# Performance work log

Hardware: AMD Instinct MI355X
Metric: run time of the kernel (lower is better)

## Reference

```python
import jax, jax.numpy as jnp
import numpy as np

B, N, K = 2, 8192, 16
C_IN, C_OUT = 32, 64
EPS = 1e-6


def _bn(x, g, b, axes):
    m = jnp.mean(x, axes, keepdims=True)
    v = jnp.var(x, axes, keepdims=True)
    return (x - m) * jax.lax.rsqrt(v + EPS) * g + b


def _leaky(x, s):
    return jnp.where(x >= 0, x, s * x)


def _knn(coords, k):
    # brute-force euclidean KNN, self point included (dist 0)
    sq = jnp.sum(coords * coords, -1)  # (B,N)
    d2 = sq[:, :, None] + sq[:, None, :] - 2.0 * jnp.einsum('bnd,bmd->bnm', coords, coords)
    neg, idx = jax.lax.top_k(-d2, k)  # (B,N,K)
    dist = jnp.sqrt(jnp.clip(-neg, 1e-12, None))
    return idx, dist


def setup_inputs() -> dict:
    key = jax.random.key(0)
    ks = jax.random.split(key, 12)
    h = C_OUT // 2
    w = lambda k, s: jax.random.normal(k, s, jnp.float32) * 0.05
    return {
        'coords': jax.random.normal(ks[0], (B, N, 3), jnp.float32),
        'features': jax.random.normal(ks[1], (B, N, C_IN), jnp.float32),
        'W_mlp1': w(ks[2], (C_IN, h)), 'b_mlp1': jnp.zeros(h, jnp.float32),
        'W_lse1': w(ks[3], (10, h)), 'b_lse1': jnp.zeros(h, jnp.float32),
        'g_lse1': jnp.ones(h, jnp.float32), 'be_lse1': jnp.zeros(h, jnp.float32),
        'W_att1_lin': w(ks[4], (C_OUT, C_OUT)),
        'W_att1_mlp': w(ks[5], (C_OUT, h)), 'b_att1_mlp': jnp.zeros(h, jnp.float32),
        'g_att1': jnp.ones(h, jnp.float32), 'be_att1': jnp.zeros(h, jnp.float32),
        'W_lse2': w(ks[6], (10, h)), 'b_lse2': jnp.zeros(h, jnp.float32),
        'g_lse2': jnp.ones(h, jnp.float32), 'be_lse2': jnp.zeros(h, jnp.float32),
        'W_att2_lin': w(ks[7], (C_OUT, C_OUT)),
        'W_att2_mlp': w(ks[8], (C_OUT, C_OUT)), 'b_att2_mlp': jnp.zeros(C_OUT, jnp.float32),
        'g_att2': jnp.ones(C_OUT, jnp.float32), 'be_att2': jnp.zeros(C_OUT, jnp.float32),
        'W_mlp2': w(ks[9], (C_OUT, 2 * C_OUT)), 'b_mlp2': jnp.zeros(2 * C_OUT, jnp.float32),
        'W_short': w(ks[10], (C_IN, 2 * C_OUT)), 'b_short': jnp.zeros(2 * C_OUT, jnp.float32),
        'g_short': jnp.ones(2 * C_OUT, jnp.float32), 'be_short': jnp.zeros(2 * C_OUT, jnp.float32),
    }


def _forward(coords, features, W_mlp1, b_mlp1, W_lse1, b_lse1, g_lse1, be_lse1,
             W_att1_lin, W_att1_mlp, b_att1_mlp, g_att1, be_att1,
             W_lse2, b_lse2, g_lse2, be_lse2,
             W_att2_lin, W_att2_mlp, b_att2_mlp, g_att2, be_att2,
             W_mlp2, b_mlp2, W_short, b_short, g_short, be_short):
    idx, dist = _knn(coords, K)                     # (B,N,K)
    nbr = jax.vmap(lambda c, i: c[i])(coords, idx)  # gather neighbor coords (B,N,K,3)
    center = jnp.broadcast_to(coords[:, :, None, :], nbr.shape)
    # spatial encoding: [center, neighbor, center-neighbor, dist] -> 10 channels
    se = jnp.concatenate([center, nbr, center - nbr, dist[..., None]], -1)  # (B,N,K,10)

    # mlp1 (1x1 conv + LeakyReLU(0.2)), no BN
    x = _leaky(features @ W_mlp1 + b_mlp1, 0.2)     # (B,N,h)

    # LocSE 1: shared MLP (BN train-mode + ReLU) on spatial enc, concat features
    sp1 = jax.nn.relu(_bn(se @ W_lse1 + b_lse1, g_lse1, be_lse1, (0, 1, 2)))  # (B,N,K,h)
    x1 = jnp.concatenate([sp1, jnp.broadcast_to(x[:, :, None, :], sp1.shape)], -1)  # (B,N,K,2h)

    # attention pooling 1: softmax over neighbors K, weighted sum, MLP+BN+ReLU
    sc1 = jax.nn.softmax(x1 @ W_att1_lin, axis=2)
    p1 = jnp.sum(sc1 * x1, axis=2)                  # (B,N,2h)
    x = jax.nn.relu(_bn(p1 @ W_att1_mlp + b_att1_mlp, g_att1, be_att1, (0, 1)))  # (B,N,h)

    # LocSE 2 + attention pooling 2 (same KNN, separate weights)
    sp2 = jax.nn.relu(_bn(se @ W_lse2 + b_lse2, g_lse2, be_lse2, (0, 1, 2)))
    x2 = jnp.concatenate([sp2, jnp.broadcast_to(x[:, :, None, :], sp2.shape)], -1)
    sc2 = jax.nn.softmax(x2 @ W_att2_lin, axis=2)
    p2 = jnp.sum(sc2 * x2, axis=2)
    x = jax.nn.relu(_bn(p2 @ W_att2_mlp + b_att2_mlp, g_att2, be_att2, (0, 1)))  # (B,N,C_OUT)

    # mlp2 (no BN, no act) + shortcut (BN, no act), residual LeakyReLU(0.01)
    x = x @ W_mlp2 + b_mlp2                          # (B,N,2*C_OUT)
    short = _bn(features @ W_short + b_short, g_short, be_short, (0, 1))
    out = _leaky(x + short, 0.01)
    # match torch layout (B, 2*C_OUT, N, 1)
    return jnp.transpose(out, (0, 2, 1))[..., None]


def reference(coords, features, W_mlp1, b_mlp1, W_lse1, b_lse1, g_lse1, be_lse1,
              W_att1_lin, W_att1_mlp, b_att1_mlp, g_att1, be_att1,
              W_lse2, b_lse2, g_lse2, be_lse2,
              W_att2_lin, W_att2_mlp, b_att2_mlp, g_att2, be_att2,
              W_mlp2, b_mlp2, W_short, b_short, g_short, be_short):
    return _forward(coords, features, W_mlp1, b_mlp1, W_lse1, b_lse1, g_lse1, be_lse1,
                    W_att1_lin, W_att1_mlp, b_att1_mlp, g_att1, be_att1,
                    W_lse2, b_lse2, g_lse2, be_lse2,
                    W_att2_lin, W_att2_mlp, b_att2_mlp, g_att2, be_att2,
                    W_mlp2, b_mlp2, W_short, b_short, g_short, be_short)
```

## Files before the change

kernel.cpp:

```cpp
#include <hip/hip_runtime.h>
#include <cfloat>
#include <cmath>

#define DEV __device__ __forceinline__

constexpr int BB = 2, NN = 8192, KK = 16, CIN = 32, HH = 32, CO = 64, C2 = 128;
constexpr int BNTOT = BB * NN;
constexpr int BNKROWS = BB * NN * KK;
constexpr float EPSF = 1e-6f;

constexpr int S_LSE1 = 0, S_LSE2 = 64, S_ATT1 = 128, S_ATT2 = 192, S_SHORT = 320, S_TOTAL = 576;
constexpr int SS_LSE1 = 0, SS_LSE2 = 64, SS_ATT1 = 128, SS_ATT2 = 192, SS_SHORT = 320, SS_TOTAL = 576;

constexpr size_t OFF_CP4   = 0;
constexpr size_t OFF_SE    = OFF_CP4 + (size_t)BNTOT * 4;
constexpr size_t OFF_XF    = OFF_SE + (size_t)BNKROWS * 10;
constexpr size_t OFF_SHORT = OFF_XF + (size_t)BNTOT * HH;
constexpr size_t OFF_PRE1  = OFF_SHORT + (size_t)BNTOT * C2;
constexpr size_t OFF_PRE2  = OFF_PRE1 + (size_t)BNTOT * HH;
constexpr size_t OFF_SS    = OFF_PRE2 + (size_t)BNTOT * CO;
constexpr size_t OFF_STATS = OFF_SS + SS_TOTAL;

__global__ __launch_bounds__(256) void k_prep(const float* __restrict__ coords,
                                              float4* __restrict__ cp4) {
#pragma clang fp contract(off)
    int i = blockIdx.x * 256 + threadIdx.x;
    if (i >= BNTOT) return;
    float x = coords[3 * i], y = coords[3 * i + 1], z = coords[3 * i + 2];
    float sq = (x * x + y * y) + z * z;
    cp4[i] = make_float4(x, y, z, sq);
}

DEV float dist2(float4 qc, float4 c) {
#pragma clang fp contract(off)
    float dot = (qc.x * c.x + qc.y * c.y) + qc.z * c.z;
    return (qc.w + c.w) - 2.0f * dot;
}

DEV unsigned encf(float f) {
    unsigned u = __float_as_uint(f);
    return (u & 0x80000000u) ? ~u : (u | 0x80000000u);
}
DEV float decf(unsigned e) {
    unsigned u = (e & 0x80000000u) ? (e & 0x7FFFFFFFu) : ~e;
    return __uint_as_float(u);
}

DEV void ins16(float (&dl)[16], int (&il)[16], float d, int id) {
    float dk = d; int jk = id;
#pragma unroll
    for (int r = 0; r < 16; ++r) {
        bool c = dk < dl[r];
        float td = dl[r]; int ti = il[r];
        dl[r] = c ? dk : dl[r]; il[r] = c ? jk : il[r];
        dk = c ? td : dk; jk = c ? ti : jk;
    }
}

DEV void ins16_lex(float (&dl)[16], int (&il)[16], float d, int id) {
    float dk = d; int jk = id;
#pragma unroll
    for (int r = 0; r < 16; ++r) {
        bool c = (dk < dl[r]) || (dk == dl[r] && jk < il[r]);
        float td = dl[r]; int ti = il[r];
        dl[r] = c ? dk : dl[r]; il[r] = c ? jk : il[r];
        dk = c ? td : dk; jk = c ? ti : jk;
    }
}

__global__ __launch_bounds__(256) void k_knn(const float4* __restrict__ cp4,
                                             float* __restrict__ se) {
    __shared__ uint2 buf[7][256];
    __shared__ float mdl[8][32][17];
    __shared__ int   mil[8][32][17];
    __shared__ unsigned thr[32];

    int t = threadIdx.x;
    int b = blockIdx.x >> 8;
    int qbase = (blockIdx.x & 255) * 32;
    int ql = t & 31, part = t >> 5;
    const float4* cp = cp4 + (size_t)b * NN;
    float4 qc = cp[qbase + ql];

    if (t < 32) thr[t] = encf(FLT_MAX);
    __syncthreads();

    float dl[16]; int il[16];
#pragma unroll
    for (int i = 0; i < 16; ++i) { dl[i] = FLT_MAX; il[i] = 0; }

    int cb = part * 1024;
#pragma unroll
    for (int k = 0; k < 16; ++k) ins16(dl, il, dist2(qc, cp[cb + k]), cb + k);
    atomicMin(&thr[ql], encf(dl[15]));
    float Tf = dl[15];
    int cnt = 0;

    float4 n0 = cp[cb + 16], n1 = cp[cb + 17], n2 = cp[cb + 18], n3 = cp[cb + 19];
    unsigned te = thr[ql];
    for (int j = cb + 16; j < cb + 1024; j += 4) {
        float4 c0 = n0, c1 = n1, c2 = n2, c3 = n3;
        n0 = cp[j + 4]; n1 = cp[j + 5]; n2 = cp[j + 6]; n3 = cp[j + 7];
        float d0 = dist2(qc, c0), d1 = dist2(qc, c1), d2v = dist2(qc, c2), d3 = dist2(qc, c3);
        bool p0 = d0 <= Tf, p1 = d1 <= Tf, p2 = d2v <= Tf, p3 = d3 <= Tf;
        if (__any(p0 | p1 | p2 | p3)) {
            if (p0) { buf[cnt][t] = make_uint2(__float_as_uint(d0), (unsigned)(j)); ++cnt; }
            if (p1) { buf[cnt][t] = make_uint2(__float_as_uint(d1), (unsigned)(j + 1)); ++cnt; }
            if (p2) { buf[cnt][t] = make_uint2(__float_as_uint(d2v), (unsigned)(j + 2)); ++cnt; }
            if (p3) { buf[cnt][t] = make_uint2(__float_as_uint(d3), (unsigned)(j + 3)); ++cnt; }
            if (__any(cnt >= 4)) {
#pragma unroll
                for (int s = 0; s < 7; ++s) {
                    if (s < cnt) {
                        uint2 v = buf[s][t];
                        float d = __uint_as_float(v.x);
                        if (d < dl[15]) ins16(dl, il, d, (int)v.y);
                    }
                }
                cnt = 0;
                atomicMin(&thr[ql], encf(dl[15]));
            }
        }
        Tf = decf(te);
        te = thr[ql];
    }
    if (__any(cnt > 0)) {
#pragma unroll
        for (int s = 0; s < 7; ++s) {
            if (s < cnt) {
                uint2 v = buf[s][t];
                float d = __uint_as_float(v.x);
                if (d < dl[15]) ins16(dl, il, d, (int)v.y);
            }
        }
    }

#pragma unroll
    for (int i = 0; i < 16; ++i) { mdl[part][ql][i] = dl[i]; mil[part][ql][i] = il[i]; }
    __syncthreads();

    for (int half = 4; half >= 1; half >>= 1) {
        if (part < half) {
#pragma unroll
            for (int i = 0; i < 16; ++i) {
                float d = mdl[part + half][ql][i]; int id = mil[part + half][ql][i];
                if (d < dl[15] || (d == dl[15] && id < il[15])) ins16_lex(dl, il, d, id);
            }
#pragma unroll
            for (int i = 0; i < 16; ++i) { mdl[part][ql][i] = dl[i]; mil[part][ql][i] = il[i]; }
        }
        __syncthreads();
    }

    for (int s = t; s < 512; s += 256) {
        int qq = s >> 4, k = s & 15;
        float d2s = mdl[0][qq][k]; int id = mil[0][qq][k];
        float4 qc2 = cp[qbase + qq];
        float4 nb = cp[id];
        float dist = sqrtf(fmaxf(d2s, 1e-12f));
        float* sp = se + ((size_t)(b * NN + qbase + qq) * KK + k) * 10;
        sp[0] = qc2.x; sp[1] = qc2.y; sp[2] = qc2.z;
        sp[3] = nb.x;  sp[4] = nb.y;  sp[5] = nb.z;
        sp[6] = qc2.x - nb.x; sp[7] = qc2.y - nb.y; sp[8] = qc2.z - nb.z;
        sp[9] = dist;
    }
}

__global__ __launch_bounds__(128) void k_feat(const float* __restrict__ feat,
                                              const float* __restrict__ Wm1, const float* __restrict__ bm1,
                                              const float* __restrict__ Wsh, const float* __restrict__ bsh,
                                              float* __restrict__ xf, float* __restrict__ short_pre,
                                              double* __restrict__ stats) {
    __shared__ float fl[32][33];
    int t = threadIdx.x;
    int pbase = blockIdx.x * 32;
    float wcol[32];
#pragma unroll
    for (int i = 0; i < 32; ++i) wcol[i] = Wsh[i * C2 + t];
    float wm[32];
    if (t < 32) {
#pragma unroll
        for (int i = 0; i < 32; ++i) wm[i] = Wm1[i * HH + t];
    }
    float bs = bsh[t];
    float bm = (t < 32) ? bm1[t] : 0.f;
    double s = 0.0, s2 = 0.0;

    for (int e = t; e < 1024; e += 128) {
        int p = e >> 5, i = e & 31;
        fl[p][i] = feat[(size_t)(pbase + p) * CIN + i];
    }
    __syncthreads();
    for (int p = 0; p < 32; ++p) {
        float acc = bs;
#pragma unroll
        for (int i = 0; i < 32; ++i) acc += fl[p][i] * wcol[i];
        int gp = pbase + p;
        short_pre[(size_t)gp * C2 + t] = acc;
        s += acc; s2 += (double)acc * acc;
        if (t < 32) {
            float xv = bm;
#pragma unroll
            for (int i = 0; i < 32; ++i) xv += fl[p][i] * wm[i];
            xf[(size_t)gp * HH + t] = xv >= 0.f ? xv : 0.2f * xv;
        }
    }
    atomicAdd(&stats[S_SHORT + t], s);
    atomicAdd(&stats[S_SHORT + C2 + t], s2);
}

__global__ __launch_bounds__(256) void k_lse_stats(const float* __restrict__ se,
                                                   const float* __restrict__ W1, const float* __restrict__ b1,
                                                   const float* __restrict__ W2, const float* __restrict__ b2,
                                                   double* __restrict__ stats) {
    __shared__ float srows[256][10];
    __shared__ double red[4][64][2];
    int t = threadIdx.x;
    int c = t & 63, grp = t >> 6;
    int ch = c & 31; bool second = c >= 32;
    const float* W = second ? W2 : W1;
    float wcol[10];
#pragma unroll
    for (int d = 0; d < 10; ++d) wcol[d] = W[d * HH + ch];
    float bb = second ? b2[ch] : b1[ch];
    double s = 0.0, s2 = 0.0;
    int rbase = blockIdx.x * 512;

    for (int tile = 0; tile < 2; ++tile) {
        __syncthreads();
        const float* src = se + (size_t)(rbase + tile * 256) * 10;
        for (int e = t; e < 2560; e += 256) srows[e / 10][e % 10] = src[e];
        __syncthreads();
        int r0 = grp * 64;
        for (int r = r0; r < r0 + 64; ++r) {
            float acc = bb;
#pragma unroll
            for (int d = 0; d < 10; ++d) acc += srows[r][d] * wcol[d];
            s += acc; s2 += (double)acc * acc;
        }
    }
    red[grp][c][0] = s; red[grp][c][1] = s2;
    __syncthreads();
    if (grp == 0) {
        for (int g = 1; g < 4; ++g) { s += red[g][c][0]; s2 += red[g][c][1]; }
        int base = second ? S_LSE2 : S_LSE1;
        atomicAdd(&stats[base + ch], s);
        atomicAdd(&stats[base + 32 + ch], s2);
    }
}

DEV void fin_one(const double* stats, int sbase, int ch, int nch, double M,
                 const float* g, const float* be, float* ss, int ssbase) {
    double mean = stats[sbase + ch] / M;
    double var = stats[sbase + nch + ch] / M - mean * mean;
    double scale = (double)g[ch] / sqrt(var + (double)EPSF);
    double shift = (double)be[ch] - mean * scale;
    ss[ssbase + ch] = (float)scale;
    ss[ssbase + nch + ch] = (float)shift;
}

__global__ void k_fin_misc(const double* __restrict__ stats, float* __restrict__ ss,
                           const float* g1, const float* be1, const float* g2, const float* be2,
                           const float* gs, const float* bes) {
    int t = threadIdx.x;
    if (t < 32) fin_one(stats, S_LSE1, t, 32, (double)BNKROWS, g1, be1, ss, SS_LSE1);
    else if (t < 64) fin_one(stats, S_LSE2, t - 32, 32, (double)BNKROWS, g2, be2, ss, SS_LSE2);
    else if (t < 192) fin_one(stats, S_SHORT, t - 64, 128, (double)BNTOT, gs, bes, ss, SS_SHORT);
}

__global__ void k_fin_att(const double* __restrict__ stats, float* __restrict__ ss,
                          const float* g, const float* be, int sbase, int nch, int ssbase) {
    int t = threadIdx.x;
    if (t < nch) fin_one(stats, sbase, t, nch, (double)BNTOT, g, be, ss, ssbase);
}

template <int OUTC, bool SECOND>
__global__ __launch_bounds__(256) void k_att(const float* __restrict__ se,
                                             const float* __restrict__ featsrc,
                                             const float* __restrict__ Wlse, const float* __restrict__ blse,
                                             const float* __restrict__ Wlin,
                                             const float* __restrict__ Wmlp, const float* __restrict__ bmlp,
                                             const float* __restrict__ ss, int lse_ss, int feat_ss, int stat_base,
                                             float* __restrict__ preout, double* __restrict__ stats) {
    __shared__ __align__(16) float wlt[64][68];
    __shared__ float wm[64][OUTC];
    __shared__ __align__(16) float x1[4][16][40];
    __shared__ float fv[4][32];
    __shared__ float p1b[4][64];
    __shared__ double red[4][OUTC][2];

    int t = threadIdx.x, w = t >> 6, c = t & 63;
    int ch = c & 31, half = c >> 5;
    for (int e = t; e < 4096; e += 256) wlt[e & 63][e >> 6] = Wlin[e];
    for (int e = t; e < 64 * OUTC; e += 256) wm[e / OUTC][e % OUTC] = Wmlp[e];

    float wf[10]; float bf;
    {
        float sc_ = ss[lse_ss + ch], sh_ = ss[lse_ss + 32 + ch];
#pragma unroll
        for (int d = 0; d < 10; ++d) wf[d] = Wlse[d * 32 + ch] * sc_;
        bf = blse[ch] * sc_ + sh_;
    }
    float fa = 1.f, fb = 0.f;
    if (SECOND && c >= 32) { fa = ss[feat_ss + ch]; fb = ss[feat_ss + 32 + ch]; }
    double s = 0.0, s2 = 0.0;
    __syncthreads();

    for (int i = 0; i < 8; ++i) {
        int p = blockIdx.x * 32 + w * 8 + i;

        int kbase = half * 8;
        const float* sp = se + (size_t)p * (KK * 10) + kbase * 10;
        float myv[8];
#pragma unroll
        for (int kk = 0; kk < 8; ++kk) {
            float acc = bf;
#pragma unroll
            for (int d = 0; d < 10; ++d) acc += sp[kk * 10 + d] * wf[d];
            myv[kk] = fmaxf(acc, 0.f);
        }
#pragma unroll
        for (int kk = 0; kk < 8; ++kk) x1[w][kbase + kk][ch] = myv[kk];

        float xv = 0.f;
        if (c >= 32) {
            xv = featsrc[(size_t)p * 32 + ch];
            if (SECOND) xv = fmaxf(xv * fa + fb, 0.f);
            fv[w][ch] = xv;
        }

        float col[16];
        if (c < 32) {
#pragma unroll
            for (int kk = 0; kk < 8; ++kk) col[kk] = myv[kk];
#pragma unroll
            for (int kk = 0; kk < 8; ++kk) col[8 + kk] = x1[w][8 + kk][ch];
        } else {
#pragma unroll
            for (int k = 0; k < 16; ++k) col[k] = xv;
        }

        float cst = 0.f;
#pragma unroll
        for (int dg = 8; dg < 16; ++dg) {
            float4 wv = *(const float4*)&wlt[c][dg * 4];
            float4 xvv = *(const float4*)&fv[w][(dg - 8) * 4];
            cst += xvv.x * wv.x + xvv.y * wv.y + xvv.z * wv.z + xvv.w * wv.w;
        }
        float scv[16];
#pragma unroll
        for (int k = 0; k < 16; ++k) scv[k] = cst;
        for (int dg = 0; dg < 8; ++dg) {
            float4 wv = *(const float4*)&wlt[c][dg * 4];
#pragma unroll
            for (int k = 0; k < 16; ++k) {
                float4 xvv = *(const float4*)&x1[w][k][dg * 4];
                scv[k] += xvv.x * wv.x + xvv.y * wv.y + xvv.z * wv.z + xvv.w * wv.w;
            }
        }
        float m = scv[0];
#pragma unroll
        for (int k = 1; k < 16; ++k) m = fmaxf(m, scv[k]);
        float sum = 0.f, p1 = 0.f;
#pragma unroll
        for (int k = 0; k < 16; ++k) { float e = __expf(scv[k] - m); sum += e; p1 += e * col[k]; }
        p1 /= sum;
        p1b[w][c] = p1;

        if (c < OUTC) {
            float acc = bmlp[c];
#pragma unroll
            for (int d = 0; d < 64; ++d) acc += p1b[w][d] * wm[d][c];
            preout[(size_t)p * OUTC + c] = acc;
            s += acc; s2 += (double)acc * acc;
        }
    }
    if (c < OUTC) { red[w][c][0] = s; red[w][c][1] = s2; }
    __syncthreads();
    if (t < OUTC) {
        double ts = red[0][t][0], ts2 = red[0][t][1];
        for (int g = 1; g < 4; ++g) { ts += red[g][t][0]; ts2 += red[g][t][1]; }
        atomicAdd(&stats[stat_base + t], ts);
        atomicAdd(&stats[stat_base + OUTC + t], ts2);
    }
}

__global__ __launch_bounds__(256) void k_out(const float* __restrict__ pre2,
                                             const float* __restrict__ short_pre,
                                             const float* __restrict__ W2, const float* __restrict__ b2,
                                             const float* __restrict__ ss, float* __restrict__ out) {
    __shared__ __align__(16) float w2[64][128];
    __shared__ float sc2[64], sh2[64], scs[128], shs[128], bb[128];
    int t = threadIdx.x;
    int pl = t & 63, seg = t >> 6;
    for (int e = t; e < 8192; e += 256) w2[e >> 7][e & 127] = W2[e];
    if (t < 64) { sc2[t] = ss[SS_ATT2 + t]; sh2[t] = ss[SS_ATT2 + 64 + t]; }
    if (t < 128) { scs[t] = ss[SS_SHORT + t]; shs[t] = ss[SS_SHORT + 128 + t]; bb[t] = b2[t]; }
    __syncthreads();

    int p = blockIdx.x * 64 + pl;
    int b = p >> 13, n = p & 8191;
    const float* pr = pre2 + (size_t)p * 64;
    float xa[64];
#pragma unroll
    for (int c = 0; c < 64; c += 4) {
        float4 v = *(const float4*)&pr[c];
        xa[c + 0] = fmaxf(v.x * sc2[c + 0] + sh2[c + 0], 0.f);
        xa[c + 1] = fmaxf(v.y * sc2[c + 1] + sh2[c + 1], 0.f);
        xa[c + 2] = fmaxf(v.z * sc2[c + 2] + sh2[c + 2], 0.f);
        xa[c + 3] = fmaxf(v.w * sc2[c + 3] + sh2[c + 3], 0.f);
    }
    const float* shp = short_pre + (size_t)p * 128;
    int obase = seg * 32;
    for (int o = obase; o < obase + 32; o += 4) {
        float a0 = bb[o], a1 = bb[o + 1], a2 = bb[o + 2], a3 = bb[o + 3];
#pragma unroll
        for (int cc = 0; cc < 64; ++cc) {
            float4 wv = *(const float4*)&w2[cc][o];
            float x = xa[cc];
            a0 += x * wv.x; a1 += x * wv.y; a2 += x * wv.z; a3 += x * wv.w;
        }
        float4 sv = *(const float4*)&shp[o];
        float r0 = a0 + (sv.x * scs[o] + shs[o]);
        float r1 = a1 + (sv.y * scs[o + 1] + shs[o + 1]);
        float r2 = a2 + (sv.z * scs[o + 2] + shs[o + 2]);
        float r3 = a3 + (sv.w * scs[o + 3] + shs[o + 3]);
        out[((size_t)(b * C2 + o + 0)) * NN + n] = r0 >= 0.f ? r0 : 0.01f * r0;
        out[((size_t)(b * C2 + o + 1)) * NN + n] = r1 >= 0.f ? r1 : 0.01f * r1;
        out[((size_t)(b * C2 + o + 2)) * NN + n] = r2 >= 0.f ? r2 : 0.01f * r2;
        out[((size_t)(b * C2 + o + 3)) * NN + n] = r3 >= 0.f ? r3 : 0.01f * r3;
    }
}

extern "C" void kernel_launch(void* const* d_in, const int* in_sizes, int n_in,
                              void* d_out, int out_size, void* d_ws, size_t ws_size,
                              hipStream_t stream) {
    const float* coords    = (const float*)d_in[0];
    const float* features  = (const float*)d_in[1];
    const float* W_mlp1    = (const float*)d_in[2];
    const float* b_mlp1    = (const float*)d_in[3];
    const float* W_lse1    = (const float*)d_in[4];
    const float* b_lse1    = (const float*)d_in[5];
    const float* g_lse1    = (const float*)d_in[6];
    const float* be_lse1   = (const float*)d_in[7];
    const float* W_att1_lin= (const float*)d_in[8];
    const float* W_att1_mlp= (const float*)d_in[9];
    const float* b_att1_mlp= (const float*)d_in[10];
    const float* g_att1    = (const float*)d_in[11];
    const float* be_att1   = (const float*)d_in[12];
    const float* W_lse2    = (const float*)d_in[13];
    const float* b_lse2    = (const float*)d_in[14];
    const float* g_lse2    = (const float*)d_in[15];
    const float* be_lse2   = (const float*)d_in[16];
    const float* W_att2_lin= (const float*)d_in[17];
    const float* W_att2_mlp= (const float*)d_in[18];
    const float* b_att2_mlp= (const float*)d_in[19];
    const float* g_att2    = (const float*)d_in[20];
    const float* be_att2   = (const float*)d_in[21];
    const float* W_mlp2    = (const float*)d_in[22];
    const float* b_mlp2    = (const float*)d_in[23];
    const float* W_short   = (const float*)d_in[24];
    const float* b_short   = (const float*)d_in[25];
    const float* g_short   = (const float*)d_in[26];
    const float* be_short  = (const float*)d_in[27];

    float* ws = (float*)d_ws;
    float4* cp4      = (float4*)(ws + OFF_CP4);
    float* se        = ws + OFF_SE;
    float* xf        = ws + OFF_XF;
    float* short_pre = ws + OFF_SHORT;
    float* pre1      = ws + OFF_PRE1;
    float* pre2      = ws + OFF_PRE2;
    float* ss        = ws + OFF_SS;
    double* stats    = (double*)(ws + OFF_STATS);
    float* out       = (float*)d_out;

    hipMemsetAsync(stats, 0, S_TOTAL * sizeof(double), stream);

    k_prep<<<BNTOT / 256, 256, 0, stream>>>(coords, cp4);
    k_knn<<<512, 256, 0, stream>>>(cp4, se);
    k_feat<<<512, 128, 0, stream>>>(features, W_mlp1, b_mlp1, W_short, b_short,
                                    xf, short_pre, stats);
    k_lse_stats<<<512, 256, 0, stream>>>(se, W_lse1, b_lse1, W_lse2, b_lse2, stats);
    k_fin_misc<<<1, 192, 0, stream>>>(stats, ss, g_lse1, be_lse1, g_lse2, be_lse2,
                                      g_short, be_short);
    k_att<32, false><<<512, 256, 0, stream>>>(se, xf, W_lse1, b_lse1, W_att1_lin,
                                              W_att1_mlp, b_att1_mlp, ss,
                                              SS_LSE1, 0, S_ATT1, pre1, stats);
    k_fin_att<<<1, 64, 0, stream>>>(stats, ss, g_att1, be_att1, S_ATT1, 32, SS_ATT1);
    k_att<64, true><<<512, 256, 0, stream>>>(se, pre1, W_lse2, b_lse2, W_att2_lin,
                                             W_att2_mlp, b_att2_mlp, ss,
                                             SS_LSE2, SS_ATT1, S_ATT2, pre2, stats);
    k_fin_att<<<1, 64, 0, stream>>>(stats, ss, g_att2, be_att2, S_ATT2, 64, SS_ATT2);
    k_out<<<BNTOT / 64, 256, 0, stream>>>(pre2, short_pre, W_mlp2, b_mlp2, ss, out);
}
```

Before: 406.9 us.

## Sort points by Morton cell and prune KNN chunks with bounding boxes

```diff
diff --git a/kernel.cpp b/kernel.cpp
--- a/kernel.cpp
+++ b/kernel.cpp
@@ -8,9 +8,10 @@
 constexpr int BNTOT = BB * NN;
 constexpr int BNKROWS = BB * NN * KK;
 constexpr float EPSF = 1e-6f;
+constexpr int NCELL = 4096;
+constexpr int NCHUNK = 128;
 
 constexpr int S_LSE1 = 0, S_LSE2 = 64, S_ATT1 = 128, S_ATT2 = 192, S_SHORT = 320, S_TOTAL = 576;
-constexpr int SS_LSE1 = 0, SS_LSE2 = 64, SS_ATT1 = 128, SS_ATT2 = 192, SS_SHORT = 320, SS_TOTAL = 576;
 
 constexpr size_t OFF_CP4   = 0;
 constexpr size_t OFF_SE    = OFF_CP4 + (size_t)BNTOT * 4;
@@ -18,17 +19,85 @@
 constexpr size_t OFF_SHORT = OFF_XF + (size_t)BNTOT * HH;
 constexpr size_t OFF_PRE1  = OFF_SHORT + (size_t)BNTOT * C2;
 constexpr size_t OFF_PRE2  = OFF_PRE1 + (size_t)BNTOT * HH;
-constexpr size_t OFF_SS    = OFF_PRE2 + (size_t)BNTOT * CO;
-constexpr size_t OFF_STATS = OFF_SS + SS_TOTAL;
+constexpr size_t OFF_STATS = OFF_PRE2 + (size_t)BNTOT * CO;
+constexpr size_t OFF_COUNTS= OFF_STATS + 2 * S_TOTAL;
+constexpr size_t OFF_CODE  = OFF_SHORT;
+constexpr size_t OFF_CPS   = OFF_CODE + 16384;
+constexpr size_t OFF_OIDX  = OFF_CPS + (size_t)BNTOT * 4 + 16;
+constexpr size_t OFF_BBOX  = OFF_OIDX + 16384;
+
+DEV unsigned spr3(unsigned v) {
+    return (v & 1u) | ((v & 2u) << 2) | ((v & 4u) << 4) | ((v & 8u) << 6);
+}
 
 __global__ __launch_bounds__(256) void k_prep(const float* __restrict__ coords,
-                                              float4* __restrict__ cp4) {
+                                              float4* __restrict__ cp4,
+                                              int* __restrict__ code, int* __restrict__ counts) {
 #pragma clang fp contract(off)
     int i = blockIdx.x * 256 + threadIdx.x;
     if (i >= BNTOT) return;
     float x = coords[3 * i], y = coords[3 * i + 1], z = coords[3 * i + 2];
     float sq = (x * x + y * y) + z * z;
     cp4[i] = make_float4(x, y, z, sq);
+    const float inv = 16.f / 8.8f;
+    int ix = min(15, max(0, (int)floorf((x + 4.4f) * inv)));
+    int iy = min(15, max(0, (int)floorf((y + 4.4f) * inv)));
+    int iz = min(15, max(0, (int)floorf((z + 4.4f) * inv)));
+    unsigned m = spr3(ix) | (spr3(iy) << 1) | (spr3(iz) << 2);
+    code[i] = (int)m;
+    atomicAdd(&counts[((i >> 13) << 12) + m], 1);
+}
+
+__global__ __launch_bounds__(256) void k_scan(int* __restrict__ counts) {
+    __shared__ int lds[256];
+    int t = threadIdx.x;
+    for (int b = 0; b < 2; ++b) {
+        int base = b * NCELL;
+        int v[16]; int s = 0;
+#pragma unroll
+        for (int k = 0; k < 16; ++k) { int tmp = counts[base + t * 16 + k]; v[k] = s; s += tmp; }
+        lds[t] = s;
+        __syncthreads();
+        for (int o = 1; o < 256; o <<= 1) {
+            int u = (t >= o) ? lds[t - o] : 0;
+            __syncthreads();
+            lds[t] += u;
+            __syncthreads();
+        }
+        int off = lds[t] - s;
+#pragma unroll
+        for (int k = 0; k < 16; ++k) counts[base + t * 16 + k] = off + v[k];
+        __syncthreads();
+    }
+}
+
+__global__ __launch_bounds__(256) void k_scatter(const float4* __restrict__ cp4,
+                                                 const int* __restrict__ code,
+                                                 int* __restrict__ cursor,
+                                                 float4* __restrict__ cps, int* __restrict__ oidx) {
+    int i = blockIdx.x * 256 + threadIdx.x;
+    if (i >= BNTOT) return;
+    int b = i >> 13, n = i & 8191;
+    int c = code[i];
+    int pos = atomicAdd(&cursor[(b << 12) + c], 1);
+    cps[(b << 13) + pos] = cp4[i];
+    oidx[(b << 13) + pos] = n;
+}
+
+__global__ __launch_bounds__(64) void k_bbox(const float4* __restrict__ cps,
+                                             float* __restrict__ bboxg) {
+    int c = blockIdx.x, lane = threadIdx.x;
+    float4 p = cps[c * 64 + lane];
+    float lox = p.x, hix = p.x, loy = p.y, hiy = p.y, loz = p.z, hiz = p.z;
+    for (int o = 32; o > 0; o >>= 1) {
+        lox = fminf(lox, __shfl_down(lox, o)); hix = fmaxf(hix, __shfl_down(hix, o));
+        loy = fminf(loy, __shfl_down(loy, o)); hiy = fmaxf(hiy, __shfl_down(hiy, o));
+        loz = fminf(loz, __shfl_down(loz, o)); hiz = fmaxf(hiz, __shfl_down(hiz, o));
+    }
+    if (lane == 0) {
+        float* bb = bboxg + c * 8;
+        bb[0] = lox; bb[1] = loy; bb[2] = loz; bb[3] = hix; bb[4] = hiy; bb[5] = hiz;
+    }
 }
 
 DEV float dist2(float4 qc, float4 c) {
@@ -37,6 +106,13 @@
     return (qc.w + c.w) - 2.0f * dot;
 }
 
+DEV float md2box(float4 q, const float* bb) {
+    float dx = fmaxf(0.f, fmaxf(bb[0] - q.x, q.x - bb[3]));
+    float dy = fmaxf(0.f, fmaxf(bb[1] - q.y, q.y - bb[4]));
+    float dz = fmaxf(0.f, fmaxf(bb[2] - q.z, q.z - bb[5]));
+    return dx * dx + dy * dy + dz * dz;
+}
+
 DEV unsigned encf(float f) {
     unsigned u = __float_as_uint(f);
     return (u & 0x80000000u) ? ~u : (u | 0x80000000u);
@@ -44,17 +120,6 @@
 DEV float decf(unsigned e) {
     unsigned u = (e & 0x80000000u) ? (e & 0x7FFFFFFFu) : ~e;
     return __uint_as_float(u);
-}
-
-DEV void ins16(float (&dl)[16], int (&il)[16], float d, int id) {
-    float dk = d; int jk = id;
-#pragma unroll
-    for (int r = 0; r < 16; ++r) {
-        bool c = dk < dl[r];
-        float td = dl[r]; int ti = il[r];
-        dl[r] = c ? dk : dl[r]; il[r] = c ? jk : il[r];
-        dk = c ? td : dk; jk = c ? ti : jk;
-    }
 }
 
 DEV void ins16_lex(float (&dl)[16], int (&il)[16], float d, int id) {
@@ -68,73 +133,126 @@
     }
 }
 
-__global__ __launch_bounds__(256) void k_knn(const float4* __restrict__ cp4,
+__global__ __launch_bounds__(256) void k_knn(const float4* __restrict__ cps,
+                                             const int* __restrict__ oidx,
+                                             const float4* __restrict__ cp4,
+                                             const float* __restrict__ bboxg,
                                              float* __restrict__ se) {
-    __shared__ uint2 buf[7][256];
-    __shared__ float mdl[8][32][17];
+    __shared__ __align__(16) float mdl[8][32][17];
     __shared__ int   mil[8][32][17];
+    __shared__ float bbx[128][8];
+    __shared__ int   order_s[8][16];
     __shared__ unsigned thr[32];
+    uint2 (*buf)[256] = reinterpret_cast<uint2(*)[256]>(&mdl[0][0][0]);
 
     int t = threadIdx.x;
     int b = blockIdx.x >> 8;
     int qbase = (blockIdx.x & 255) * 32;
     int ql = t & 31, part = t >> 5;
-    const float4* cp = cp4 + (size_t)b * NN;
-    float4 qc = cp[qbase + ql];
-
+    const float4* cb_ = cps + ((size_t)b << 13);
+    const int* ob_ = oidx + (b << 13);
+    float4 qc = cb_[qbase + ql];
+
+    for (int e = t; e < 1024; e += 256) ((float*)bbx)[e] = bboxg[(b << 10) + e];
     if (t < 32) thr[t] = encf(FLT_MAX);
     __syncthreads();
 
+    if (ql == 0) {
+        float4 qcen = cb_[qbase + 16];
+        float md[16];
+#pragma unroll
+        for (int s = 0; s < 16; ++s) md[s] = md2box(qcen, &bbx[part * 16 + s][0]);
+        unsigned used = 0;
+        for (int s = 0; s < 16; ++s) {
+            float best = FLT_MAX; int bi = 0;
+#pragma unroll
+            for (int k = 0; k < 16; ++k) {
+                bool ok = !((used >> k) & 1u) && md[k] < best;
+                best = ok ? md[k] : best; bi = ok ? k : bi;
+            }
+            used |= 1u << bi;
+            order_s[part][s] = part * 16 + bi;
+        }
+    }
+    __syncthreads();
+
     float dl[16]; int il[16];
 #pragma unroll
-    for (int i = 0; i < 16; ++i) { dl[i] = FLT_MAX; il[i] = 0; }
-
-    int cb = part * 1024;
-#pragma unroll
-    for (int k = 0; k < 16; ++k) ins16(dl, il, dist2(qc, cp[cb + k]), cb + k);
+    for (int i = 0; i < 16; ++i) { dl[i] = FLT_MAX; il[i] = 0x7fffffff; }
+
+    int c0 = order_s[part][0];
+    {
+        int j0 = c0 * 64;
+#pragma unroll
+        for (int k = 0; k < 16; ++k) {
+            float d = dist2(qc, cb_[j0 + k]);
+            int o = ob_[j0 + k];
+            if (d < dl[15] || (d == dl[15] && o < il[15])) ins16_lex(dl, il, d, o);
+        }
+    }
     atomicMin(&thr[ql], encf(dl[15]));
     float Tf = dl[15];
+    unsigned te = thr[ql];
     int cnt = 0;
 
-    float4 n0 = cp[cb + 16], n1 = cp[cb + 17], n2 = cp[cb + 18], n3 = cp[cb + 19];
-    unsigned te = thr[ql];
-    for (int j = cb + 16; j < cb + 1024; j += 4) {
-        float4 c0 = n0, c1 = n1, c2 = n2, c3 = n3;
-        n0 = cp[j + 4]; n1 = cp[j + 5]; n2 = cp[j + 6]; n3 = cp[j + 7];
-        float d0 = dist2(qc, c0), d1 = dist2(qc, c1), d2v = dist2(qc, c2), d3 = dist2(qc, c3);
-        bool p0 = d0 <= Tf, p1 = d1 <= Tf, p2 = d2v <= Tf, p3 = d3 <= Tf;
-        if (__any(p0 | p1 | p2 | p3)) {
-            if (p0) { buf[cnt][t] = make_uint2(__float_as_uint(d0), (unsigned)(j)); ++cnt; }
-            if (p1) { buf[cnt][t] = make_uint2(__float_as_uint(d1), (unsigned)(j + 1)); ++cnt; }
-            if (p2) { buf[cnt][t] = make_uint2(__float_as_uint(d2v), (unsigned)(j + 2)); ++cnt; }
-            if (p3) { buf[cnt][t] = make_uint2(__float_as_uint(d3), (unsigned)(j + 3)); ++cnt; }
-            if (__any(cnt >= 4)) {
-#pragma unroll
-                for (int s = 0; s < 7; ++s) {
-                    if (s < cnt) {
-                        uint2 v = buf[s][t];
-                        float d = __uint_as_float(v.x);
-                        if (d < dl[15]) ins16(dl, il, d, (int)v.y);
+    for (int s = 0; s < 16; ++s) {
+        int c = order_s[part][s];
+        float md2v = md2box(qc, &bbx[c][0]);
+        bool need = md2v <= Tf * 1.001f + 1e-3f;
+        if (__any(need)) {
+            int jb = c * 64 + (s == 0 ? 16 : 0);
+            int je = c * 64 + 64;
+            float4 n0 = cb_[jb], n1 = cb_[jb + 1], n2 = cb_[jb + 2], n3 = cb_[jb + 3];
+            for (int j = jb; j < je; j += 4) {
+                float4 c0_ = n0, c1_ = n1, c2_ = n2, c3_ = n3;
+                n0 = cb_[j + 4]; n1 = cb_[j + 5]; n2 = cb_[j + 6]; n3 = cb_[j + 7];
+                float d0 = dist2(qc, c0_), d1 = dist2(qc, c1_), d2v = dist2(qc, c2_), d3 = dist2(qc, c3_);
+                bool p0 = d0 <= Tf, p1 = d1 <= Tf, p2 = d2v <= Tf, p3 = d3 <= Tf;
+                if (__any(p0 | p1 | p2 | p3)) {
+                    if (p0) { buf[cnt][t] = make_uint2(__float_as_uint(d0), (unsigned)j); ++cnt; }
+                    if (p1) { buf[cnt][t] = make_uint2(__float_as_uint(d1), (unsigned)(j + 1)); ++cnt; }
+                    if (p2) { buf[cnt][t] = make_uint2(__float_as_uint(d2v), (unsigned)(j + 2)); ++cnt; }
+                    if (p3) { buf[cnt][t] = make_uint2(__float_as_uint(d3), (unsigned)(j + 3)); ++cnt; }
+                    if (__any(cnt >= 4)) {
+                        unsigned jj[7]; int oid[7];
+#pragma unroll
+                        for (int q2 = 0; q2 < 7; ++q2) jj[q2] = (q2 < cnt) ? buf[q2][t].y : 0u;
+#pragma unroll
+                        for (int q2 = 0; q2 < 7; ++q2) oid[q2] = ob_[jj[q2]];
+#pragma unroll
+                        for (int q2 = 0; q2 < 7; ++q2) {
+                            if (q2 < cnt) {
+                                float d = __uint_as_float(buf[q2][t].x); int o = oid[q2];
+                                if (d < dl[15] || (d == dl[15] && o < il[15])) ins16_lex(dl, il, d, o);
+                            }
+                        }
+                        cnt = 0;
+                        atomicMin(&thr[ql], encf(dl[15]));
                     }
                 }
-                cnt = 0;
-                atomicMin(&thr[ql], encf(dl[15]));
+                Tf = fminf(Tf, decf(te));
+                te = thr[ql];
             }
         }
-        Tf = decf(te);
+        Tf = fminf(Tf, decf(te));
         te = thr[ql];
     }
     if (__any(cnt > 0)) {
-#pragma unroll
-        for (int s = 0; s < 7; ++s) {
-            if (s < cnt) {
-                uint2 v = buf[s][t];
-                float d = __uint_as_float(v.x);
-                if (d < dl[15]) ins16(dl, il, d, (int)v.y);
+        unsigned jj[7]; int oid[7];
+#pragma unroll
+        for (int q2 = 0; q2 < 7; ++q2) jj[q2] = (q2 < cnt) ? buf[q2][t].y : 0u;
+#pragma unroll
+        for (int q2 = 0; q2 < 7; ++q2) oid[q2] = ob_[jj[q2]];
+#pragma unroll
+        for (int q2 = 0; q2 < 7; ++q2) {
+            if (q2 < cnt) {
+                float d = __uint_as_float(buf[q2][t].x); int o = oid[q2];
+                if (d < dl[15] || (d == dl[15] && o < il[15])) ins16_lex(dl, il, d, o);
             }
         }
     }
 
+    __syncthreads();
 #pragma unroll
     for (int i = 0; i < 16; ++i) { mdl[part][ql][i] = dl[i]; mil[part][ql][i] = il[i]; }
     __syncthreads();
@@ -152,13 +270,14 @@
         __syncthreads();
     }
 
-    for (int s = t; s < 512; s += 256) {
-        int qq = s >> 4, k = s & 15;
-        float d2s = mdl[0][qq][k]; int id = mil[0][qq][k];
-        float4 qc2 = cp[qbase + qq];
-        float4 nb = cp[id];
+    for (int s2 = t; s2 < 512; s2 += 256) {
+        int qq = s2 >> 4, k = s2 & 15;
+        float d2s = mdl[0][qq][k]; int oid = mil[0][qq][k];
+        float4 qc2 = cb_[qbase + qq];
+        int oq = ob_[qbase + qq];
+        float4 nb = cp4[(b << 13) + oid];
         float dist = sqrtf(fmaxf(d2s, 1e-12f));
-        float* sp = se + ((size_t)(b * NN + qbase + qq) * KK + k) * 10;
+        float* sp = se + ((size_t)(b * NN + oq) * KK + k) * 10;
         sp[0] = qc2.x; sp[1] = qc2.y; sp[2] = qc2.z;
         sp[3] = nb.x;  sp[4] = nb.y;  sp[5] = nb.z;
         sp[6] = qc2.x - nb.x; sp[7] = qc2.y - nb.y; sp[8] = qc2.z - nb.z;
@@ -249,29 +368,12 @@
     }
 }
 
-DEV void fin_one(const double* stats, int sbase, int ch, int nch, double M,
-                 const float* g, const float* be, float* ss, int ssbase) {
+DEV float2 fin_pair(const double* stats, int sbase, int ch, int nch, double M,
+                    const float* g, const float* be) {
     double mean = stats[sbase + ch] / M;
     double var = stats[sbase + nch + ch] / M - mean * mean;
-    double scale = (double)g[ch] / sqrt(var + (double)EPSF);
-    double shift = (double)be[ch] - mean * scale;
-    ss[ssbase + ch] = (float)scale;
-    ss[ssbase + nch + ch] = (float)shift;
-}
-
-__global__ void k_fin_misc(const double* __restrict__ stats, float* __restrict__ ss,
-                           const float* g1, const float* be1, const float* g2, const float* be2,
-                           const float* gs, const float* bes) {
-    int t = threadIdx.x;
-    if (t < 32) fin_one(stats, S_LSE1, t, 32, (double)BNKROWS, g1, be1, ss, SS_LSE1);
-    else if (t < 64) fin_one(stats, S_LSE2, t - 32, 32, (double)BNKROWS, g2, be2, ss, SS_LSE2);
-    else if (t < 192) fin_one(stats, S_SHORT, t - 64, 128, (double)BNTOT, gs, bes, ss, SS_SHORT);
-}
-
-__global__ void k_fin_att(const double* __restrict__ stats, float* __restrict__ ss,
-                          const float* g, const float* be, int sbase, int nch, int ssbase) {
-    int t = threadIdx.x;
-    if (t < nch) fin_one(stats, sbase, t, nch, (double)BNTOT, g, be, ss, ssbase);
+    double scd = (double)g[ch] / sqrt(var + (double)EPSF);
+    return make_float2((float)scd, (float)((double)be[ch] - mean * scd));
 }
 
 template <int OUTC, bool SECOND>
@@ -280,8 +382,10 @@
                                              const float* __restrict__ Wlse, const float* __restrict__ blse,
                                              const float* __restrict__ Wlin,
                                              const float* __restrict__ Wmlp, const float* __restrict__ bmlp,
-                                             const float* __restrict__ ss, int lse_ss, int feat_ss, int stat_base,
-                                             float* __restrict__ preout, double* __restrict__ stats) {
+                                             double* __restrict__ stats, int lse_sbase, int feat_sbase, int stat_base,
+                                             const float* __restrict__ g_lse, const float* __restrict__ be_lse,
+                                             const float* __restrict__ g_f, const float* __restrict__ be_f,
+                                             float* __restrict__ preout) {
     __shared__ __align__(16) float wlt[64][68];
     __shared__ float wm[64][OUTC];
     __shared__ __align__(16) float x1[4][16][40];
@@ -296,13 +400,16 @@
 
     float wf[10]; float bf;
     {
-        float sc_ = ss[lse_ss + ch], sh_ = ss[lse_ss + 32 + ch];
-#pragma unroll
-        for (int d = 0; d < 10; ++d) wf[d] = Wlse[d * 32 + ch] * sc_;
-        bf = blse[ch] * sc_ + sh_;
+        float2 p = fin_pair(stats, lse_sbase, ch, 32, (double)BNKROWS, g_lse, be_lse);
+#pragma unroll
+        for (int d = 0; d < 10; ++d) wf[d] = Wlse[d * 32 + ch] * p.x;
+        bf = blse[ch] * p.x + p.y;
     }
     float fa = 1.f, fb = 0.f;
-    if (SECOND && c >= 32) { fa = ss[feat_ss + ch]; fb = ss[feat_ss + 32 + ch]; }
+    if (SECOND && c >= 32) {
+        float2 p = fin_pair(stats, feat_sbase, ch, 32, (double)BNTOT, g_f, be_f);
+        fa = p.x; fb = p.y;
+    }
     double s = 0.0, s2 = 0.0;
     __syncthreads();
 
@@ -388,14 +495,18 @@
 __global__ __launch_bounds__(256) void k_out(const float* __restrict__ pre2,
                                              const float* __restrict__ short_pre,
                                              const float* __restrict__ W2, const float* __restrict__ b2,
-                                             const float* __restrict__ ss, float* __restrict__ out) {
+                                             const double* __restrict__ stats,
+                                             const float* __restrict__ g_a2, const float* __restrict__ be_a2,
+                                             const float* __restrict__ g_s, const float* __restrict__ be_s,
+                                             float* __restrict__ out) {
     __shared__ __align__(16) float w2[64][128];
     __shared__ float sc2[64], sh2[64], scs[128], shs[128], bb[128];
     int t = threadIdx.x;
     int pl = t & 63, seg = t >> 6;
     for (int e = t; e < 8192; e += 256) w2[e >> 7][e & 127] = W2[e];
-    if (t < 64) { sc2[t] = ss[SS_ATT2 + t]; sh2[t] = ss[SS_ATT2 + 64 + t]; }
-    if (t < 128) { scs[t] = ss[SS_SHORT + t]; shs[t] = ss[SS_SHORT + 128 + t]; bb[t] = b2[t]; }
+    if (t < 64) { float2 p = fin_pair(stats, S_ATT2, t, 64, (double)BNTOT, g_a2, be_a2); sc2[t] = p.x; sh2[t] = p.y; }
+    if (t >= 64 && t < 192) { int ch = t - 64; float2 p = fin_pair(stats, S_SHORT, ch, 128, (double)BNTOT, g_s, be_s); scs[ch] = p.x; shs[ch] = p.y; }
+    if (t < 128) bb[t] = b2[t];
     __syncthreads();
 
     int p = blockIdx.x * 64 + pl;
@@ -471,26 +582,32 @@
     float* short_pre = ws + OFF_SHORT;
     float* pre1      = ws + OFF_PRE1;
     float* pre2      = ws + OFF_PRE2;
-    float* ss        = ws + OFF_SS;
     double* stats    = (double*)(ws + OFF_STATS);
+    int* counts      = (int*)(ws + OFF_COUNTS);
+    int* code        = (int*)(ws + OFF_CODE);
+    float4* cps      = (float4*)(ws + OFF_CPS);
+    int* oidxArr     = (int*)(ws + OFF_OIDX);
+    float* bboxg     = ws + OFF_BBOX;
     float* out       = (float*)d_out;
 
-    hipMemsetAsync(stats, 0, S_TOTAL * sizeof(double), stream);
-
-    k_prep<<<BNTOT / 256, 256, 0, stream>>>(coords, cp4);
-    k_knn<<<512, 256, 0, stream>>>(cp4, se);
+    hipMemsetAsync(stats, 0, S_TOTAL * 8 + 2 * NCELL * 4, stream);
+
+    k_prep<<<BNTOT / 256, 256, 0, stream>>>(coords, cp4, code, counts);
+    k_scan<<<1, 256, 0, stream>>>(counts);
+    k_scatter<<<BNTOT / 256, 256, 0, stream>>>(cp4, code, counts, cps, oidxArr);
+    k_bbox<<<BB * NCHUNK, 64, 0, stream>>>(cps, bboxg);
+    k_knn<<<512, 256, 0, stream>>>(cps, oidxArr, cp4, bboxg, se);
     k_feat<<<512, 128, 0, stream>>>(features, W_mlp1, b_mlp1, W_short, b_short,
                                     xf, short_pre, stats);
     k_lse_stats<<<512, 256, 0, stream>>>(se, W_lse1, b_lse1, W_lse2, b_lse2, stats);
-    k_fin_misc<<<1, 192, 0, stream>>>(stats, ss, g_lse1, be_lse1, g_lse2, be_lse2,
-                                      g_short, be_short);
     k_att<32, false><<<512, 256, 0, stream>>>(se, xf, W_lse1, b_lse1, W_att1_lin,
-                                              W_att1_mlp, b_att1_mlp, ss,
-                                              SS_LSE1, 0, S_ATT1, pre1, stats);
-    k_fin_att<<<1, 64, 0, stream>>>(stats, ss, g_att1, be_att1, S_ATT1, 32, SS_ATT1);
+                                              W_att1_mlp, b_att1_mlp, stats,
+                                              S_LSE1, 0, S_ATT1,
+                                              g_lse1, be_lse1, nullptr, nullptr, pre1);
     k_att<64, true><<<512, 256, 0, stream>>>(se, pre1, W_lse2, b_lse2, W_att2_lin,
-                                             W_att2_mlp, b_att2_mlp, ss,
-                                             SS_LSE2, SS_ATT1, S_ATT2, pre2, stats);
-    k_fin_att<<<1, 64, 0, stream>>>(stats, ss, g_att2, be_att2, S_ATT2, 64, SS_ATT2);
-    k_out<<<BNTOT / 64, 256, 0, stream>>>(pre2, short_pre, W_mlp2, b_mlp2, ss, out);
-}
+                                             W_att2_mlp, b_att2_mlp, stats,
+                                             S_LSE2, S_ATT1, S_ATT2,
+                                             g_lse2, be_lse2, g_att1, be_att1, pre2);
+    k_out<<<BNTOT / 64, 256, 0, stream>>>(pre2, short_pre, W_mlp2, b_mlp2, stats,
+                                          g_att2, be_att2, g_short, be_short, out);
+}
```

New measurement: 646.6 us. 1.59x slower.

## Fold BN finalize kernels into consumers and alias KNN merge buffer in LDS

Applied to the files above, without the earlier changes.

```diff
diff --git a/kernel.cpp b/kernel.cpp
--- a/kernel.cpp
+++ b/kernel.cpp
@@ -10,7 +10,6 @@
 constexpr float EPSF = 1e-6f;
 
 constexpr int S_LSE1 = 0, S_LSE2 = 64, S_ATT1 = 128, S_ATT2 = 192, S_SHORT = 320, S_TOTAL = 576;
-constexpr int SS_LSE1 = 0, SS_LSE2 = 64, SS_ATT1 = 128, SS_ATT2 = 192, SS_SHORT = 320, SS_TOTAL = 576;
 
 constexpr size_t OFF_CP4   = 0;
 constexpr size_t OFF_SE    = OFF_CP4 + (size_t)BNTOT * 4;
@@ -18,8 +17,7 @@
 constexpr size_t OFF_SHORT = OFF_XF + (size_t)BNTOT * HH;
 constexpr size_t OFF_PRE1  = OFF_SHORT + (size_t)BNTOT * C2;
 constexpr size_t OFF_PRE2  = OFF_PRE1 + (size_t)BNTOT * HH;
-constexpr size_t OFF_SS    = OFF_PRE2 + (size_t)BNTOT * CO;
-constexpr size_t OFF_STATS = OFF_SS + SS_TOTAL;
+constexpr size_t OFF_STATS = OFF_PRE2 + (size_t)BNTOT * CO;
 
 __global__ __launch_bounds__(256) void k_prep(const float* __restrict__ coords,
                                               float4* __restrict__ cp4) {
@@ -70,10 +68,10 @@
 
 __global__ __launch_bounds__(256) void k_knn(const float4* __restrict__ cp4,
                                              float* __restrict__ se) {
-    __shared__ uint2 buf[7][256];
     __shared__ float mdl[8][32][17];
     __shared__ int   mil[8][32][17];
     __shared__ unsigned thr[32];
+    uint2 (*buf)[256] = reinterpret_cast<uint2(*)[256]>(&mdl[0][0][0]);
 
     int t = threadIdx.x;
     int b = blockIdx.x >> 8;
@@ -135,6 +133,7 @@
         }
     }
 
+    __syncthreads();
 #pragma unroll
     for (int i = 0; i < 16; ++i) { mdl[part][ql][i] = dl[i]; mil[part][ql][i] = il[i]; }
     __syncthreads();
@@ -249,29 +248,12 @@
     }
 }
 
-DEV void fin_one(const double* stats, int sbase, int ch, int nch, double M,
-                 const float* g, const float* be, float* ss, int ssbase) {
+DEV float2 fin_pair(const double* stats, int sbase, int ch, int nch, double M,
+                    const float* g, const float* be) {
     double mean = stats[sbase + ch] / M;
     double var = stats[sbase + nch + ch] / M - mean * mean;
-    double scale = (double)g[ch] / sqrt(var + (double)EPSF);
-    double shift = (double)be[ch] - mean * scale;
-    ss[ssbase + ch] = (float)scale;
-    ss[ssbase + nch + ch] = (float)shift;
-}
-
-__global__ void k_fin_misc(const double* __restrict__ stats, float* __restrict__ ss,
-                           const float* g1, const float* be1, const float* g2, const float* be2,
-                           const float* gs, const float* bes) {
-    int t = threadIdx.x;
-    if (t < 32) fin_one(stats, S_LSE1, t, 32, (double)BNKROWS, g1, be1, ss, SS_LSE1);
-    else if (t < 64) fin_one(stats, S_LSE2, t - 32, 32, (double)BNKROWS, g2, be2, ss, SS_LSE2);
-    else if (t < 192) fin_one(stats, S_SHORT, t - 64, 128, (double)BNTOT, gs, bes, ss, SS_SHORT);
-}
-
-__global__ void k_fin_att(const double* __restrict__ stats, float* __restrict__ ss,
-                          const float* g, const float* be, int sbase, int nch, int ssbase) {
-    int t = threadIdx.x;
-    if (t < nch) fin_one(stats, sbase, t, nch, (double)BNTOT, g, be, ss, ssbase);
+    double scd = (double)g[ch] / sqrt(var + (double)EPSF);
+    return make_float2((float)scd, (float)((double)be[ch] - mean * scd));
 }
 
 template <int OUTC, bool SECOND>
@@ -280,8 +262,10 @@
                                              const float* __restrict__ Wlse, const float* __restrict__ blse,
                                              const float* __restrict__ Wlin,
                                              const float* __restrict__ Wmlp, const float* __restrict__ bmlp,
-                                             const float* __restrict__ ss, int lse_ss, int feat_ss, int stat_base,
-                                             float* __restrict__ preout, double* __restrict__ stats) {
+                                             double* __restrict__ stats, int lse_sbase, int feat_sbase, int stat_base,
+                                             const float* __restrict__ g_lse, const float* __restrict__ be_lse,
+                                             const float* __restrict__ g_f, const float* __restrict__ be_f,
+                                             float* __restrict__ preout) {
     __shared__ __align__(16) float wlt[64][68];
     __shared__ float wm[64][OUTC];
     __shared__ __align__(16) float x1[4][16][40];
@@ -296,13 +280,16 @@
 
     float wf[10]; float bf;
     {
-        float sc_ = ss[lse_ss + ch], sh_ = ss[lse_ss + 32 + ch];
-#pragma unroll
-        for (int d = 0; d < 10; ++d) wf[d] = Wlse[d * 32 + ch] * sc_;
-        bf = blse[ch] * sc_ + sh_;
+        float2 p = fin_pair(stats, lse_sbase, ch, 32, (double)BNKROWS, g_lse, be_lse);
+#pragma unroll
+        for (int d = 0; d < 10; ++d) wf[d] = Wlse[d * 32 + ch] * p.x;
+        bf = blse[ch] * p.x + p.y;
     }
     float fa = 1.f, fb = 0.f;
-    if (SECOND && c >= 32) { fa = ss[feat_ss + ch]; fb = ss[feat_ss + 32 + ch]; }
+    if (SECOND && c >= 32) {
+        float2 p = fin_pair(stats, feat_sbase, ch, 32, (double)BNTOT, g_f, be_f);
+        fa = p.x; fb = p.y;
+    }
     double s = 0.0, s2 = 0.0;
     __syncthreads();
 
@@ -388,14 +375,18 @@
 __global__ __launch_bounds__(256) void k_out(const float* __restrict__ pre2,
                                              const float* __restrict__ short_pre,
                                              const float* __restrict__ W2, const float* __restrict__ b2,
-                                             const float* __restrict__ ss, float* __restrict__ out) {
+                                             const double* __restrict__ stats,
+                                             const float* __restrict__ g_a2, const float* __restrict__ be_a2,
+                                             const float* __restrict__ g_s, const float* __restrict__ be_s,
+                                             float* __restrict__ out) {
     __shared__ __align__(16) float w2[64][128];
     __shared__ float sc2[64], sh2[64], scs[128], shs[128], bb[128];
     int t = threadIdx.x;
     int pl = t & 63, seg = t >> 6;
     for (int e = t; e < 8192; e += 256) w2[e >> 7][e & 127] = W2[e];
-    if (t < 64) { sc2[t] = ss[SS_ATT2 + t]; sh2[t] = ss[SS_ATT2 + 64 + t]; }
-    if (t < 128) { scs[t] = ss[SS_SHORT + t]; shs[t] = ss[SS_SHORT + 128 + t]; bb[t] = b2[t]; }
+    if (t < 64) { float2 p = fin_pair(stats, S_ATT2, t, 64, (double)BNTOT, g_a2, be_a2); sc2[t] = p.x; sh2[t] = p.y; }
+    if (t >= 64 && t < 192) { int ch = t - 64; float2 p = fin_pair(stats, S_SHORT, ch, 128, (double)BNTOT, g_s, be_s); scs[ch] = p.x; shs[ch] = p.y; }
+    if (t < 128) bb[t] = b2[t];
     __syncthreads();
 
     int p = blockIdx.x * 64 + pl;
@@ -471,7 +462,6 @@
     float* short_pre = ws + OFF_SHORT;
     float* pre1      = ws + OFF_PRE1;
     float* pre2      = ws + OFF_PRE2;
-    float* ss        = ws + OFF_SS;
     double* stats    = (double*)(ws + OFF_STATS);
     float* out       = (float*)d_out;
 
@@ -482,15 +472,14 @@
     k_feat<<<512, 128, 0, stream>>>(features, W_mlp1, b_mlp1, W_short, b_short,
                                     xf, short_pre, stats);
     k_lse_stats<<<512, 256, 0, stream>>>(se, W_lse1, b_lse1, W_lse2, b_lse2, stats);
-    k_fin_misc<<<1, 192, 0, stream>>>(stats, ss, g_lse1, be_lse1, g_lse2, be_lse2,
-                                      g_short, be_short);
     k_att<32, false><<<512, 256, 0, stream>>>(se, xf, W_lse1, b_lse1, W_att1_lin,
-                                              W_att1_mlp, b_att1_mlp, ss,
-                                              SS_LSE1, 0, S_ATT1, pre1, stats);
-    k_fin_att<<<1, 64, 0, stream>>>(stats, ss, g_att1, be_att1, S_ATT1, 32, SS_ATT1);
+                                              W_att1_mlp, b_att1_mlp, stats,
+                                              S_LSE1, 0, S_ATT1,
+                                              g_lse1, be_lse1, nullptr, nullptr, pre1);
     k_att<64, true><<<512, 256, 0, stream>>>(se, pre1, W_lse2, b_lse2, W_att2_lin,
-                                             W_att2_mlp, b_att2_mlp, ss,
-                                             SS_LSE2, SS_ATT1, S_ATT2, pre2, stats);
-    k_fin_att<<<1, 64, 0, stream>>>(stats, ss, g_att2, be_att2, S_ATT2, 64, SS_ATT2);
-    k_out<<<BNTOT / 64, 256, 0, stream>>>(pre2, short_pre, W_mlp2, b_mlp2, ss, out);
-}
+                                             W_att2_mlp, b_att2_mlp, stats,
+                                             S_LSE2, S_ATT1, S_ATT2,
+                                             g_lse2, be_lse2, g_att1, be_att1, pre2);
+    k_out<<<BNTOT / 64, 256, 0, stream>>>(pre2, short_pre, W_mlp2, b_mlp2, stats,
+                                          g_att2, be_att2, g_short, be_short, out);
+}
```

Result: no change. 403.3 us (-0.9%).
